# Performance work log

Measured on AMD Instinct MI355X. Metric: run time of the kernel, lower is better.

Reference implementation:

```python
import jax, jax.numpy as jnp
import numpy as np

B, S, D, NH, NKV, HD, FF = 2, 2048, 2048, 16, 8, 128, 8192
EPS = 1e-6
ROPE_THETA = 10000.0


def rmsnorm(x, w):
    return x * jax.lax.rsqrt(jnp.mean(x * x, axis=-1, keepdims=True) + EPS) * w


def rotate_half(x):
    h = x.shape[-1] // 2
    return jnp.concatenate([-x[..., h:], x[..., :h]], axis=-1)


def setup_inputs() -> dict:
    key = jax.random.key(0)
    ks = jax.random.split(key, 32)
    sc = 0.02
    inp = {}
    inp['x'] = jax.random.normal(ks[0], (B, S, D), dtype=jnp.float32)
    pos = jnp.arange(S, dtype=jnp.float32)
    inv = 1.0 / (ROPE_THETA ** (jnp.arange(0, HD, 2, dtype=jnp.float32) / HD))
    fr = jnp.outer(pos, inv)
    emb = jnp.concatenate([fr, fr], axis=-1)  # [S, HD]
    inp['cos'] = jnp.broadcast_to(jnp.cos(emb)[None], (B, S, HD)).astype(jnp.float32)
    inp['sin'] = jnp.broadcast_to(jnp.sin(emb)[None], (B, S, HD)).astype(jnp.float32)
    inp['vision_token_mask'] = jax.random.randint(ks[1], (B, S), 0, 2) > 0
    inp['attn_norm_w'] = jnp.ones((D,), jnp.float32)
    inp['ffn_norm_w'] = jnp.ones((D,), jnp.float32)
    shapes = {
        'wq': (D, NH * HD), 'wk': (D, NKV * HD), 'wv': (D, NKV * HD), 'wo': (NH * HD, D),
        'mm_wq': (D, NH * HD), 'mm_wk': (D, NKV * HD), 'mm_wv': (D, NKV * HD), 'mm_wo': (NH * HD, D),
        'gate_w': (D, FF), 'up_w': (D, FF), 'down_w': (FF, D),
        'mm_gate_w': (D, FF), 'mm_up_w': (D, FF), 'mm_down_w': (FF, D),
    }
    for i, (name, shp) in enumerate(shapes.items()):
        inp[name] = jax.random.normal(ks[2 + i], shp, dtype=jnp.float32) * sc
    for name in ['q_norm_w', 'k_norm_w', 'mm_q_norm_w', 'mm_k_norm_w']:
        inp[name] = jnp.ones((HD,), jnp.float32)
    return inp


def gpt_block(x, cos, sin, mask, attn_norm_w, ffn_norm_w,
              wq, wk, wv, wo, mm_wq, mm_wk, mm_wv, mm_wo,
              q_norm_w, k_norm_w, mm_q_norm_w, mm_k_norm_w,
              gate_w, up_w, down_w, mm_gate_w, mm_up_w, mm_down_w):
    m2 = mask[..., None]            # [B,S,1]
    m4 = mask[:, :, None, None]     # [B,S,1,1]
    h = rmsnorm(x, attn_norm_w)
    # dual-path QKV: text tokens use plain weights, vision tokens use mm_* weights
    q_t = rmsnorm((h @ wq).reshape(B, S, NH, HD), q_norm_w)
    q_v = rmsnorm((h @ mm_wq).reshape(B, S, NH, HD), mm_q_norm_w)
    q = jnp.where(m4, q_v, q_t)
    k_t = rmsnorm((h @ wk).reshape(B, S, NKV, HD), k_norm_w)
    k_v = rmsnorm((h @ mm_wk).reshape(B, S, NKV, HD), mm_k_norm_w)
    k = jnp.where(m4, k_v, k_t)
    v = jnp.where(m2, h @ mm_wv, h @ wv).reshape(B, S, NKV, HD)
    # RoPE (unsqueeze over head dim)
    cu = cos[:, :, None, :]
    su = sin[:, :, None, :]
    q = q * cu + rotate_half(q) * su
    k = k * cu + rotate_half(k) * su
    # GQA repeat + causal attention
    rep = NH // NKV
    k_r = jnp.repeat(k, rep, axis=2)
    v_r = jnp.repeat(v, rep, axis=2)
    scale = 1.0 / jnp.sqrt(jnp.float32(HD))
    scores = jnp.einsum('bqhd,bkhd->bhqk', q, k_r) * scale
    causal = jnp.tril(jnp.ones((S, S), bool))
    scores = jnp.where(causal, scores, jnp.float32(-1e30))
    p = jax.nn.softmax(scores, axis=-1)
    attn = jnp.einsum('bhqk,bkhd->bqhd', p, v_r).reshape(B, S, NH * HD)
    attn_out = jnp.where(m2, attn @ mm_wo, attn @ wo)
    h2 = x + attn_out
    # dual-path SwiGLU FFN
    g = rmsnorm(h2, ffn_norm_w)
    ff_t = (jax.nn.silu(g @ gate_w) * (g @ up_w)) @ down_w
    ff_v = (jax.nn.silu(g @ mm_gate_w) * (g @ mm_up_w)) @ mm_down_w
    return h2 + jnp.where(m2, ff_v, ff_t)


def reference(x, cos, sin, vision_token_mask, attn_norm_w, ffn_norm_w,
              wq, wk, wv, wo, mm_wq, mm_wk, mm_wv, mm_wo,
              q_norm_w, k_norm_w, mm_q_norm_w, mm_k_norm_w,
              gate_w, up_w, down_w, mm_gate_w, mm_up_w, mm_down_w):
    return gpt_block(x, cos, sin, vision_token_mask, attn_norm_w, ffn_norm_w,
                     wq, wk, wv, wo, mm_wq, mm_wk, mm_wv, mm_wo,
                     q_norm_w, k_norm_w, mm_q_norm_w, mm_k_norm_w,
                     gate_w, up_w, down_w, mm_gate_w, mm_up_w, mm_down_w)
```

## Files before the change

### kernel.cpp

```cpp
#include <hip/hip_runtime.h>

typedef unsigned short u16;
typedef __bf16 bf16x8 __attribute__((ext_vector_type(8)));
typedef float f32x4 __attribute__((ext_vector_type(4)));

__device__ __forceinline__ u16 f2bf(float f) {
    unsigned u = __builtin_bit_cast(unsigned, f);
    u += 0x7fffu + ((u >> 16) & 1u);
    return (u16)(u >> 16);
}
__device__ __forceinline__ float bf2f(u16 v) {
    unsigned u = ((unsigned)v) << 16;
    return __builtin_bit_cast(float, u);
}
__device__ __forceinline__ void glds16(const void* g, void* l) {
    __builtin_amdgcn_global_load_lds(
        (const __attribute__((address_space(1))) unsigned*)g,
        (__attribute__((address_space(3))) unsigned*)l, 16, 0, 0);
}

__device__ __forceinline__ void xcd_map(int bid, int nloc, int TM, int& tm, int& tn)
{
    const int xcd = bid & 7;
    int l = bid >> 3;
    const int per = nloc << 3;
    const int fullC = TM >> 3;
    const int lFull = fullC * per;
    int c, tn_l, tmIn;
    if (l < lFull) { c = l / per; int r = l - c * per; tn_l = r >> 3; tmIn = r & 7; }
    else { int r = l - lFull; int sc = TM - (fullC << 3); c = fullC; tn_l = r / sc; tmIn = r % sc; }
    tm = (c << 3) + tmIn;
    tn = xcd * nloc + tn_l;
}

__global__ __launch_bounds__(1024) void build_perm(
    const int* __restrict__ mask, int* __restrict__ perm, int* __restrict__ counts)
{
    __shared__ int sc[1024];
    int t = threadIdx.x;
    int m[4], cnt = 0;
#pragma unroll
    for (int j = 0; j < 4; j++) {
        m[j] = mask[t * 4 + j] != 0;
        cnt += (m[j] == 0);
    }
    sc[t] = cnt;
    __syncthreads();
    for (int off = 1; off < 1024; off <<= 1) {
        int v = (t >= off) ? sc[t - off] : 0;
        __syncthreads();
        sc[t] += v;
        __syncthreads();
    }
    int totT = sc[1023];
    int exT = sc[t] - cnt;
    int exV = t * 4 - exT;
    int pT = exT, pV = totT + exV;
#pragma unroll
    for (int j = 0; j < 4; j++) {
        if (m[j] == 0) perm[pT++] = t * 4 + j;
        else           perm[pV++] = t * 4 + j;
    }
    if (t == 0) { counts[0] = totT; counts[1] = 4096 - totT; }
}

__global__ __launch_bounds__(256) void transpose_bf16(
    const float* __restrict__ W, u16* __restrict__ Wt, int Kd, int Nd)
{
    __shared__ float tile[32][33];
    int k0 = blockIdx.x * 32, n0 = blockIdx.y * 32;
    int tx = threadIdx.x, ty = threadIdx.y;
#pragma unroll
    for (int i = 0; i < 32; i += 8)
        tile[ty + i][tx] = W[(long)(k0 + ty + i) * Nd + n0 + tx];
    __syncthreads();
#pragma unroll
    for (int i = 0; i < 32; i += 8)
        Wt[(long)(n0 + ty + i) * Kd + k0 + tx] = f2bf(tile[tx][ty + i]);
}

__global__ __launch_bounds__(256) void rms_x(
    const float* __restrict__ x, const float* __restrict__ w, u16* __restrict__ out)
{
    long row = blockIdx.x;
    int t = threadIdx.x, wave = t >> 6, lane = t & 63;
    const float4* x4 = (const float4*)(x + row * 2048);
    float4 a = x4[2 * t], b = x4[2 * t + 1];
    float ss = a.x*a.x + a.y*a.y + a.z*a.z + a.w*a.w
             + b.x*b.x + b.y*b.y + b.z*b.z + b.w*b.w;
#pragma unroll
    for (int m = 1; m < 64; m <<= 1) ss += __shfl_xor(ss, m);
    __shared__ float red[4];
    if (lane == 0) red[wave] = ss;
    __syncthreads();
    float tot = red[0] + red[1] + red[2] + red[3];
    float inv = rsqrtf(tot * (1.0f / 2048.0f) + 1e-6f);
    const float4* w4 = (const float4*)w;
    float4 wa = w4[2 * t], wb = w4[2 * t + 1];
    u16* op = out + row * 2048 + t * 8;
    op[0] = f2bf(a.x * inv * wa.x); op[1] = f2bf(a.y * inv * wa.y);
    op[2] = f2bf(a.z * inv * wa.z); op[3] = f2bf(a.w * inv * wa.w);
    op[4] = f2bf(b.x * inv * wb.x); op[5] = f2bf(b.y * inv * wb.y);
    op[6] = f2bf(b.z * inv * wb.z); op[7] = f2bf(b.w * inv * wb.w);
}

template <int EPI, bool PG, bool PC>
__global__ __launch_bounds__(512, 4) void gemm32(
    const u16* __restrict__ A, const u16* __restrict__ Bt0, const u16* __restrict__ Bt1,
    void* __restrict__ Cv,
    const int* __restrict__ perm, const int* __restrict__ counts, int N, int K)
{
    extern __shared__ u16 lds[];
    int tm, tn;
    xcd_map(blockIdx.x, N >> 11, 33, tm, tn);
    const int nT = counts[0];
    const int tT = (nT + 127) >> 7, tV = (4096 - nT + 127) >> 7;
    if (tm >= tT + tV) return;
    const bool vis = tm >= tT;
    const u16* Bt = vis ? Bt1 : Bt0;
    const int rowbase = vis ? nT + (tm - tT) * 128 : tm * 128;
    const int rowlim = vis ? 4096 : nT;
    const int tid = threadIdx.x;
    const int wave = tid >> 6, lane = tid & 63;
    const int wrbase = (wave >> 2) * 64, wcbase = (wave & 3) * 64;
    const int lr = lane & 15, lg = lane >> 4;
    const int n0 = tn * 256;
    const int t4 = tid >> 2, sp = tid & 3;
    const char* aSrc;
    const char* bSrc[2];
    {
        int r = t4;
        int gr = rowbase + r; gr = gr < 4095 ? gr : 4095;
        long ar = PG ? perm[gr] : gr;
        aSrc = (const char*)A + ar * (long)K * 2 + ((sp ^ (r & 3)) << 4);
    }
#pragma unroll
    for (int c = 0; c < 2; c++) {
        int r = c * 128 + t4;
        bSrc[c] = (const char*)Bt + (long)(n0 + r) * K * 2 + ((sp ^ (r & 3)) << 4);
    }
    auto stage = [&](int kt, int bu) {
        char* ab = (char*)lds + bu * 24576;
        long ko = (long)kt * 64;
        glds16(aSrc + ko, ab + tid * 16);
#pragma unroll
        for (int c = 0; c < 2; c++)
            glds16(bSrc[c] + ko, ab + 8192 + c * 8192 + tid * 16);
    };
    auto ldA = [&](int bu, int mi) -> bf16x8 {
        const char* ab = (const char*)lds + bu * 24576;
        int row = wrbase + mi * 16 + lr;
        return *(const bf16x8*)(ab + row * 64 + ((lg ^ (row & 3)) << 4));
    };
    auto ldB = [&](int bu, int ni) -> bf16x8 {
        const char* bb = (const char*)lds + bu * 24576 + 8192;
        int row = wcbase + ni * 16 + lr;
        return *(const bf16x8*)(bb + row * 64 + ((lg ^ (row & 3)) << 4));
    };

    f32x4 acc[4][4] = {};
    const int nkt = K >> 5;
    stage(0, 0);
    stage(1, 1);
    for (int kt = 0; kt < nkt; ++kt) {
        const int bu = kt % 3;
        if (kt == nkt - 1) asm volatile("s_waitcnt vmcnt(0)" ::: "memory");
        else               asm volatile("s_waitcnt vmcnt(3)" ::: "memory");
        __builtin_amdgcn_s_barrier();
        if (kt + 2 < nkt) stage(kt + 2, (kt + 2) % 3);
        bf16x8 af[4], bq[4];
#pragma unroll
        for (int i = 0; i < 4; i++) af[i] = ldA(bu, i);
#pragma unroll
        for (int j = 0; j < 4; j++) bq[j] = ldB(bu, j);
        __builtin_amdgcn_s_setprio(1);
#pragma unroll
        for (int i = 0; i < 4; i++)
#pragma unroll
            for (int j = 0; j < 4; j++)
                acc[i][j] = __builtin_amdgcn_mfma_f32_16x16x32_bf16(
                    af[i], bq[j], acc[i][j], 0, 0, 0);
        __builtin_amdgcn_s_setprio(0);
    }
#pragma unroll
    for (int mi = 0; mi < 4; mi++)
#pragma unroll
        for (int r = 0; r < 4; r++) {
            int gr = rowbase + wrbase + mi * 16 + lg * 4 + r;
            if (gr >= rowlim) continue;
            long crow = PC ? (long)perm[gr] : (long)gr;
#pragma unroll
            for (int ni = 0; ni < 4; ni++) {
                long col = n0 + wcbase + ni * 16 + lr;
                ((u16*)Cv)[crow * (long)N + col] = f2bf(acc[mi][ni][r]);
            }
        }
}

__global__ __launch_bounds__(512, 4) void gemm_gu(
    const u16* __restrict__ A,
    const u16* __restrict__ Bg0, const u16* __restrict__ Bg1,
    const u16* __restrict__ Bu0, const u16* __restrict__ Bu1,
    u16* __restrict__ C,
    const int* __restrict__ perm, const int* __restrict__ counts, int N, int K)
{
    extern __shared__ u16 lds[];
    int tm, tn;
    xcd_map(blockIdx.x, N >> 10, 33, tm, tn);
    const int nT = counts[0];
    const int tT = (nT + 127) >> 7, tV = (4096 - nT + 127) >> 7;
    if (tm >= tT + tV) return;
    const bool vis = tm >= tT;
    const u16* Bg = vis ? Bg1 : Bg0;
    const u16* Bu = vis ? Bu1 : Bu0;
    const int rowbase = vis ? nT + (tm - tT) * 128 : tm * 128;
    const int rowlim = vis ? 4096 : nT;
    const int tid = threadIdx.x;
    const int wave = tid >> 6, lane = tid & 63;
    const int wrbase = (wave >> 2) * 64, wcbase = (wave & 3) * 32;
    const int lr = lane & 15, lg = lane >> 4;
    const int n0 = tn * 128;
    const int t4 = tid >> 2, sp = tid & 3;
    const char *aSrc, *gSrc, *uSrc;
    {
        int r = t4;
        int gr = rowbase + r; gr = gr < 4095 ? gr : 4095;
        long ar = (long)perm[gr];
        aSrc = (const char*)A + ar * (long)K * 2 + ((sp ^ (r & 3)) << 4);
        gSrc = (const char*)Bg + (long)(n0 + r) * K * 2 + ((sp ^ (r & 3)) << 4);
        uSrc = (const char*)Bu + (long)(n0 + r) * K * 2 + ((sp ^ (r & 3)) << 4);
    }
    auto stage = [&](int kt, int bu) {
        char* ab = (char*)lds + bu * 24576;
        long ko = (long)kt * 64;
        glds16(aSrc + ko, ab + tid * 16);
        glds16(gSrc + ko, ab + 8192 + tid * 16);
        glds16(uSrc + ko, ab + 16384 + tid * 16);
    };
    auto ldA = [&](int bu, int mi) -> bf16x8 {
        const char* ab = (const char*)lds + bu * 24576;
        int row = wrbase + mi * 16 + lr;
        return *(const bf16x8*)(ab + row * 64 + ((lg ^ (row & 3)) << 4));
    };
    auto ldGU = [&](int bu, int sub, int ni) -> bf16x8 {
        const char* p = (const char*)lds + bu * 24576 + 8192 + sub * 8192;
        int row = wcbase + ni * 16 + lr;
        return *(const bf16x8*)(p + row * 64 + ((lg ^ (row & 3)) << 4));
    };

    f32x4 accg[4][2] = {}, accu[4][2] = {};
    const int nkt = K >> 5;
    stage(0, 0);
    stage(1, 1);
    for (int kt = 0; kt < nkt; ++kt) {
        const int bu = kt % 3;
        if (kt == nkt - 1) asm volatile("s_waitcnt vmcnt(0)" ::: "memory");
        else               asm volatile("s_waitcnt vmcnt(3)" ::: "memory");
        __builtin_amdgcn_s_barrier();
        if (kt + 2 < nkt) stage(kt + 2, (kt + 2) % 3);
        bf16x8 af[4], bg[2], bv[2];
#pragma unroll
        for (int i = 0; i < 4; i++) af[i] = ldA(bu, i);
#pragma unroll
        for (int j = 0; j < 2; j++) {
            bg[j] = ldGU(bu, 0, j);
            bv[j] = ldGU(bu, 1, j);
        }
        __builtin_amdgcn_s_setprio(1);
#pragma unroll
        for (int i = 0; i < 4; i++)
#pragma unroll
            for (int j = 0; j < 2; j++) {
                accg[i][j] = __builtin_amdgcn_mfma_f32_16x16x32_bf16(
                    af[i], bg[j], accg[i][j], 0, 0, 0);
                accu[i][j] = __builtin_amdgcn_mfma_f32_16x16x32_bf16(
                    af[i], bv[j], accu[i][j], 0, 0, 0);
            }
        __builtin_amdgcn_s_setprio(0);
    }
#pragma unroll
    for (int mi = 0; mi < 4; mi++)
#pragma unroll
        for (int r = 0; r < 4; r++) {
            int gr = rowbase + wrbase + mi * 16 + lg * 4 + r;
            if (gr >= rowlim) continue;
#pragma unroll
            for (int ni = 0; ni < 2; ni++) {
                long col = n0 + wcbase + ni * 16 + lr;
                float g = accg[mi][ni][r], u = accu[mi][ni][r];
                C[(long)gr * N + col] = f2bf(g / (1.0f + __expf(-g)) * u);
            }
        }
}

template <int EPI, bool PG, bool PC>
__global__ __launch_bounds__(512, 2) void gemmk(
    const u16* __restrict__ A, const u16* __restrict__ Bt0, const u16* __restrict__ Bt1,
    void* __restrict__ Cv, const float* __restrict__ resid,
    const int* __restrict__ perm, const int* __restrict__ counts, int N, int K)
{
    extern __shared__ u16 lds[];
    int tm, tn;
    xcd_map(blockIdx.x, N >> 11, 33, tm, tn);
    const int nT = counts[0];
    const int tT = (nT + 127) >> 7, tV = (4096 - nT + 127) >> 7;
    if (tm >= tT + tV) return;
    const bool vis = tm >= tT;
    const u16* Bt = vis ? Bt1 : Bt0;
    const int rowbase = vis ? nT + (tm - tT) * 128 : tm * 128;
    const int rowlim = vis ? 4096 : nT;
    const int tid = threadIdx.x;
    const int wave = tid >> 6, lane = tid & 63;
    const int wrbase = (wave >> 2) * 64, wcbase = (wave & 3) * 64;
    const int lr = lane & 15, lg = lane >> 4;
    const int n0 = tn * 256;
    const int t8 = tid >> 3, sp = tid & 7;
    const char* aSrc[2];
    const char* bSrc[4];
#pragma unroll
    for (int c = 0; c < 2; c++) {
        int r = c * 64 + t8;
        int gr = rowbase + r; gr = gr < 4095 ? gr : 4095;
        long ar = PG ? perm[gr] : gr;
        aSrc[c] = (const char*)A + ar * (long)K * 2 + ((sp ^ (r & 7)) << 4);
    }
#pragma unroll
    for (int c = 0; c < 4; c++) {
        int r = c * 64 + t8;
        bSrc[c] = (const char*)Bt + (long)(n0 + r) * K * 2 + ((sp ^ (r & 7)) << 4);
    }
    auto stage = [&](int kt, int bu) {
        char* ab = (char*)lds + bu * 49152;
        char* bb = ab + 16384;
        long ko = (long)kt * 128;
#pragma unroll
        for (int c = 0; c < 2; c++)
            glds16(aSrc[c] + ko, ab + c * 8192 + tid * 16);
#pragma unroll
        for (int c = 0; c < 4; c++)
            glds16(bSrc[c] + ko, bb + c * 8192 + tid * 16);
    };
    auto ldA = [&](int bu, int mi, int kk) -> bf16x8 {
        const char* ab = (const char*)lds + bu * 49152;
        int row = wrbase + mi * 16 + lr;
        int sl = kk * 4 + lg;
        return *(const bf16x8*)(ab + row * 128 + ((sl ^ (row & 7)) << 4));
    };
    auto ldB = [&](int bu, int ni, int kk) -> bf16x8 {
        const char* bb = (const char*)lds + bu * 49152 + 16384;
        int row = wcbase + ni * 16 + lr;
        int sl = kk * 4 + lg;
        return *(const bf16x8*)(bb + row * 128 + ((sl ^ (row & 7)) << 4));
    };

    f32x4 acc[4][4] = {};
    const int nkt = K >> 6;
    stage(0, 0);
    stage(1, 1);
    for (int kt = 0; kt < nkt; ++kt) {
        const int bu = kt % 3;
        if (kt == nkt - 1) asm volatile("s_waitcnt vmcnt(0)" ::: "memory");
        else               asm volatile("s_waitcnt vmcnt(6)" ::: "memory");
        __builtin_amdgcn_s_barrier();
        if (kt + 2 < nkt) stage(kt + 2, (kt + 2) % 3);
#pragma unroll
        for (int kk = 0; kk < 2; kk++) {
            bf16x8 af[4], bq[4];
#pragma unroll
            for (int i = 0; i < 4; i++) af[i] = ldA(bu, i, kk);
#pragma unroll
            for (int j = 0; j < 4; j++) bq[j] = ldB(bu, j, kk);
            __builtin_amdgcn_s_setprio(1);
#pragma unroll
            for (int i = 0; i < 4; i++)
#pragma unroll
                for (int j = 0; j < 4; j++)
                    acc[i][j] = __builtin_amdgcn_mfma_f32_16x16x32_bf16(
                        af[i], bq[j], acc[i][j], 0, 0, 0);
            __builtin_amdgcn_s_setprio(0);
        }
    }
#pragma unroll
    for (int mi = 0; mi < 4; mi++)
#pragma unroll
        for (int r = 0; r < 4; r++) {
            int gr = rowbase + wrbase + mi * 16 + lg * 4 + r;
            if (gr >= rowlim) continue;
            long crow = PC ? (long)perm[gr] : (long)gr;
#pragma unroll
            for (int ni = 0; ni < 4; ni++) {
                long col = n0 + wcbase + ni * 16 + lr;
                long idx = crow * (long)N + col;
                float v = acc[mi][ni][r];
                if (EPI == 1)      ((u16*)Cv)[idx] = f2bf(v);
                else if (EPI == 2) ((float*)Cv)[idx] = resid[idx] + v;
            }
        }
}

__global__ __launch_bounds__(256) void qk_fuse(
    const u16* __restrict__ p, const int* __restrict__ mask,
    const float* __restrict__ cs, const float* __restrict__ sn,
    const float* __restrict__ nwt, const float* __restrict__ nwv,
    u16* __restrict__ out, int H, int stride)
{
    int wave = threadIdx.x >> 6, lane = threadIdx.x & 63;
    int gw = blockIdx.x * 4 + wave;
    int tok = gw / H, h = gw % H;
    int b = tok >> 11, s = tok & 2047;
    const u16* src = p + (long)tok * stride + h * 128;
    const float* w = mask[tok] ? nwv : nwt;
    int d = lane * 2;
    float yx = bf2f(src[d]), yy = bf2f(src[d + 1]);
    float ss = yx * yx + yy * yy;
#pragma unroll
    for (int m = 1; m < 64; m <<= 1) ss += __shfl_xor(ss, m);
    float inv = rsqrtf(ss * (1.0f / 128.0f) + 1e-6f);
    float y0 = yx * inv * w[d], y1 = yy * inv * w[d + 1];
    float o0 = __shfl_xor(y0, 32), o1 = __shfl_xor(y1, 32);
    float sgn = (lane < 32) ? -1.0f : 1.0f;
    const float* cp = cs + (long)tok * 128 + d;
    const float* sp = sn + (long)tok * 128 + d;
    float r0 = y0 * cp[0] + sgn * o0 * sp[0];
    float r1 = y1 * cp[1] + sgn * o1 * sp[1];
    u16* op = out + (((long)b * H + h) * 2048 + s) * 128 + d;
    op[0] = f2bf(r0); op[1] = f2bf(r1);
}

__global__ __launch_bounds__(256) void v_fuse(
    const u16* __restrict__ vsrc, u16* __restrict__ outv, int stride)
{
    __shared__ u16 tile[32][33];
    int s0 = blockIdx.x * 32, d0 = blockIdx.y * 32;
    int bkv = blockIdx.z, b = bkv >> 3, kv = bkv & 7;
    int tx = threadIdx.x, ty = threadIdx.y;
#pragma unroll
    for (int i = 0; i < 32; i += 8) {
        long tok = (long)b * 2048 + s0 + ty + i;
        tile[ty + i][tx] = vsrc[tok * stride + kv * 128 + d0 + tx];
    }
    __syncthreads();
#pragma unroll
    for (int i = 0; i < 32; i += 8)
        outv[(((long)b * 8 + kv) * 128 + d0 + ty + i) * 2048 + s0 + tx] =
            tile[tx][ty + i];
}

__global__ __launch_bounds__(256) void attn_fwd(
    const u16* __restrict__ q, const u16* __restrict__ k,
    const u16* __restrict__ v, u16* __restrict__ out)
{
    __shared__ u16 Ks[32 * 128];
    __shared__ u16 Vs[128 * 32];
    __shared__ u16 Ps[4][16][40];
    const int tid = threadIdx.x, wave = tid >> 6, lane = tid & 63;
    const int lr = lane & 15, lg = lane >> 4;
    const int b = blockIdx.z, h = blockIdx.y, q0 = blockIdx.x * 64;
    const int kvh = h >> 1;
    const u16* qp = q + (((long)b * 16 + h) * 2048 + q0 + wave * 16) * 128;
    bf16x8 qf[4];
#pragma unroll
    for (int f = 0; f < 4; f++)
        qf[f] = *(const bf16x8*)(qp + (long)lr * 128 + f * 32 + lg * 8);
    const char* kbase = (const char*)(k + ((long)b * 8 + kvh) * 2048 * 128);
    const char* vbase = (const char*)(v + ((long)b * 8 + kvh) * 128 * 2048);
    f32x4 o[8] = {};
    float lsum[4] = {};
    const float sc2 = 0.08838834764831845f * 1.44269504088896f;
    const float MB = 16.5f;
    const int ntiles = (q0 + 64) >> 5;
    for (int t = 0; t < ntiles; ++t) {
        int kv0 = t * 32;
        __syncthreads();
#pragma unroll
        for (int j = 0; j < 2; j++) {
            int L = (j * 4 + wave) * 1024 + lane * 16;
            {
                int row = L >> 8, cb = L & 255;
                glds16(kbase + (long)(kv0 + row) * 256 + (cb ^ ((row & 7) << 4)),
                       (char*)Ks + (j * 4 + wave) * 1024);
            }
            {
                int row = L >> 6, cb = L & 63;
                glds16(vbase + (long)row * 4096 + kv0 * 2 + (cb ^ ((row & 3) << 4)),
                       (char*)Vs + (j * 4 + wave) * 1024);
            }
        }
        __syncthreads();
        f32x4 s[2] = {};
#pragma unroll
        for (int sub = 0; sub < 2; ++sub)
#pragma unroll
            for (int f = 0; f < 4; ++f) {
                int row = sub * 16 + lr;
                int cb = (f * 64 + lg * 16) ^ ((row & 7) << 4);
                bf16x8 kf = *(const bf16x8*)((const char*)Ks + row * 256 + cb);
                s[sub] = __builtin_amdgcn_mfma_f32_16x16x32_bf16(qf[f], kf, s[sub], 0, 0, 0);
            }
#pragma unroll
        for (int r = 0; r < 4; r++) {
            int rowg = q0 + wave * 16 + lg * 4 + r;
            float s0 = s[0][r] * sc2 - MB; if (kv0 + lr > rowg)      s0 = -1e30f;
            float s1 = s[1][r] * sc2 - MB; if (kv0 + 16 + lr > rowg) s1 = -1e30f;
            float p0 = exp2f(s0), p1 = exp2f(s1);
            lsum[r] += p0 + p1;
            int prow = lg * 4 + r;
            Ps[wave][prow][lr] = f2bf(p0);
            Ps[wave][prow][16 + lr] = f2bf(p1);
        }
        bf16x8 pf = *(const bf16x8*)&Ps[wave][lr][lg * 8];
#pragma unroll
        for (int ni = 0; ni < 8; ni++) {
            int row = ni * 16 + lr;
            int cb = (lg * 16) ^ ((row & 3) << 4);
            bf16x8 vf = *(const bf16x8*)((const char*)Vs + row * 64 + cb);
            o[ni] = __builtin_amdgcn_mfma_f32_16x16x32_bf16(pf, vf, o[ni], 0, 0, 0);
        }
    }
#pragma unroll
    for (int r = 0; r < 4; r++)
#pragma unroll
        for (int mm = 1; mm < 16; mm <<= 1) lsum[r] += __shfl_xor(lsum[r], mm);
#pragma unroll
    for (int ni = 0; ni < 8; ni++)
#pragma unroll
        for (int r = 0; r < 4; r++) {
            long row = (long)b * 2048 + q0 + wave * 16 + lg * 4 + r;
            out[row * 2048 + h * 128 + ni * 16 + lr] = f2bf(o[ni][r] / lsum[r]);
        }
}

extern "C" void kernel_launch(void* const* d_in, const int* in_sizes, int n_in,
                              void* d_out, int out_size, void* d_ws, size_t ws_size,
                              hipStream_t stream)
{
    const float* x    = (const float*)d_in[0];
    const float* cosp = (const float*)d_in[1];
    const float* sinp = (const float*)d_in[2];
    const int*   mask = (const int*)d_in[3];
    const float* anw  = (const float*)d_in[4];
    const float* fnw  = (const float*)d_in[5];
    const float* wq   = (const float*)d_in[6];
    const float* wk   = (const float*)d_in[7];
    const float* wv   = (const float*)d_in[8];
    const float* wo   = (const float*)d_in[9];
    const float* mwq  = (const float*)d_in[10];
    const float* mwk  = (const float*)d_in[11];
    const float* mwv  = (const float*)d_in[12];
    const float* mwo  = (const float*)d_in[13];
    const float* gw   = (const float*)d_in[14];
    const float* uw   = (const float*)d_in[15];
    const float* dw   = (const float*)d_in[16];
    const float* mgw  = (const float*)d_in[17];
    const float* muw  = (const float*)d_in[18];
    const float* mdw  = (const float*)d_in[19];
    const float* qnw  = (const float*)d_in[20];
    const float* knw  = (const float*)d_in[21];
    const float* mqnw = (const float*)d_in[22];
    const float* mknw = (const float*)d_in[23];

    char* base = (char*)d_ws;
    u16* wA0   = (u16*)(base);
    u16* wA1   = (u16*)(base + (32u << 20));
    u16* wB0   = (u16*)(base + (64u << 20));
    u16* wB1   = (u16*)(base + (96u << 20));
    u16* hbf   = (u16*)(base + (64u << 20));
    u16* qkv   = (u16*)(base + (80u << 20));
    u16* qb    = (u16*)(base + (112u << 20));
    u16* kb    = (u16*)(base + (128u << 20));
    u16* vb    = (u16*)(base + (136u << 20));
    u16* attnb = (u16*)(base + (144u << 20));
    u16* e1    = (u16*)(base + (128u << 20));
    float* h2  = (float*)(base + (192u << 20));
    u16* gbf   = (u16*)(base + (224u << 20));
    int* perm  = (int*)(base + (240u << 20));
    int* cnts  = perm + 4096;

    hipFuncSetAttribute((const void*)&gemm32<1, true, true>,
                        hipFuncAttributeMaxDynamicSharedMemorySize, 73728);
    hipFuncSetAttribute((const void*)&gemm_gu,
                        hipFuncAttributeMaxDynamicSharedMemorySize, 73728);
    hipFuncSetAttribute((const void*)&gemmk<2, true, true>,
                        hipFuncAttributeMaxDynamicSharedMemorySize, 147456);
    hipFuncSetAttribute((const void*)&gemmk<2, false, true>,
                        hipFuncAttributeMaxDynamicSharedMemorySize, 147456);

    dim3 tb(32, 8);
    auto TR = [&](const float* w, u16* dst, int K, int N) {
        transpose_bf16<<<dim3(K / 32, N / 32), tb, 0, stream>>>(w, dst, K, N);
    };

    build_perm<<<1, 1024, 0, stream>>>(mask, perm, cnts);
    rms_x<<<4096, 256, 0, stream>>>(x, anw, hbf);

    TR(wq, wA0, 2048, 2048);
    TR(wk, wA0 + (long)2048 * 2048, 2048, 1024);
    TR(wv, wA0 + (long)3072 * 2048, 2048, 1024);
    TR(mwq, wA1, 2048, 2048);
    TR(mwk, wA1 + (long)2048 * 2048, 2048, 1024);
    TR(mwv, wA1 + (long)3072 * 2048, 2048, 1024);
    gemm32<1, true, true><<<528, 512, 73728, stream>>>(
        hbf, wA0, wA1, (void*)qkv, perm, cnts, 4096, 2048);

    qk_fuse<<<16384, 256, 0, stream>>>(qkv, mask, cosp, sinp, qnw, mqnw, qb, 16, 4096);
    qk_fuse<<<8192, 256, 0, stream>>>(qkv + 2048, mask, cosp, sinp, knw, mknw, kb, 8, 4096);
    v_fuse<<<dim3(64, 4, 16), tb, 0, stream>>>(qkv + 3072, vb, 4096);

    attn_fwd<<<dim3(32, 16, 2), 256, 0, stream>>>(qb, kb, vb, attnb);

    TR(wo, wA0, 2048, 2048); TR(mwo, wA1, 2048, 2048);
    gemmk<2, true, true><<<264, 512, 147456, stream>>>(
        attnb, wA0, wA1, (void*)h2, x, perm, cnts, 2048, 2048);

    rms_x<<<4096, 256, 0, stream>>>(h2, fnw, gbf);

    TR(gw, wA0, 2048, 8192); TR(mgw, wA1, 2048, 8192);
    TR(uw, wB0, 2048, 8192); TR(muw, wB1, 2048, 8192);
    gemm_gu<<<2112, 512, 73728, stream>>>(
        gbf, wA0, wA1, wB0, wB1, e1, perm, cnts, 8192, 2048);
    TR(dw, wA0, 8192, 2048); TR(mdw, wA1, 8192, 2048);
    gemmk<2, false, true><<<264, 512, 147456, stream>>>(
        e1, wA0, wA1, (void*)d_out, h2, perm, cnts, 2048, 8192);
}
```

Measured before the change: 1.118 ms.

## Vectorize weight transpose and use smaller-tile GEMM for down projection

The fp32-to-bf16 weight transpose now works on 64x64 tiles, loading float4 and storing 8 packed bf16 values per thread, to cut memory transactions. The down-projection GEMM moves from the large-tile gemmk kernel to a new gemmsq kernel. gemmsq uses 128x128 tiles, double-buffered 32 KB of LDS, a K-step of 32 and an occupancy hint of 4 blocks, and is launched with twice as many blocks. This is meant to fill the GPU better for N=2048. The trade-off is less data reuse per tile and more global traffic for the K=8192 reduction.

```diff
diff --git a/kernel.cpp b/kernel.cpp
--- a/kernel.cpp
+++ b/kernel.cpp
@@ -67,16 +67,28 @@
 __global__ __launch_bounds__(256) void transpose_bf16(
     const float* __restrict__ W, u16* __restrict__ Wt, int Kd, int Nd)
 {
-    __shared__ float tile[32][33];
-    int k0 = blockIdx.x * 32, n0 = blockIdx.y * 32;
-    int tx = threadIdx.x, ty = threadIdx.y;
-#pragma unroll
-    for (int i = 0; i < 32; i += 8)
-        tile[ty + i][tx] = W[(long)(k0 + ty + i) * Nd + n0 + tx];
+    __shared__ float tile[64][65];
+    int k0 = blockIdx.x * 64, n0 = blockIdx.y * 64;
+    int t = threadIdx.x;
+    int rr = t >> 4, cc = (t & 15) * 4;
+#pragma unroll
+    for (int i = 0; i < 4; i++) {
+        float4 v = *(const float4*)&W[(long)(k0 + i * 16 + rr) * Nd + n0 + cc];
+        tile[i * 16 + rr][cc]     = v.x;
+        tile[i * 16 + rr][cc + 1] = v.y;
+        tile[i * 16 + rr][cc + 2] = v.z;
+        tile[i * 16 + rr][cc + 3] = v.w;
+    }
     __syncthreads();
-#pragma unroll
-    for (int i = 0; i < 32; i += 8)
-        Wt[(long)(n0 + ty + i) * Kd + k0 + tx] = f2bf(tile[tx][ty + i]);
+    int nn = t >> 3, k8 = (t & 7) * 8;
+#pragma unroll
+    for (int i = 0; i < 2; i++) {
+        int n = i * 32 + nn;
+        u16 pk[8];
+#pragma unroll
+        for (int j = 0; j < 8; j++) pk[j] = f2bf(tile[k8 + j][n]);
+        *(uint4*)&Wt[(long)(n0 + n) * Kd + k0 + k8] = *(const uint4*)pk;
+    }
 }
 
 __global__ __launch_bounds__(256) void rms_x(
@@ -294,6 +306,90 @@
 }
 
 template <int EPI, bool PG, bool PC>
+__global__ __launch_bounds__(512, 4) void gemmsq(
+    const u16* __restrict__ A, const u16* __restrict__ Bt0, const u16* __restrict__ Bt1,
+    void* __restrict__ Cv, const float* __restrict__ resid,
+    const int* __restrict__ perm, const int* __restrict__ counts, int N, int K)
+{
+    extern __shared__ u16 lds[];
+    int tm, tn;
+    xcd_map(blockIdx.x, N >> 10, 33, tm, tn);
+    const int nT = counts[0];
+    const int tT = (nT + 127) >> 7, tV = (4096 - nT + 127) >> 7;
+    if (tm >= tT + tV) return;
+    const bool vis = tm >= tT;
+    const u16* Bt = vis ? Bt1 : Bt0;
+    const int rowbase = vis ? nT + (tm - tT) * 128 : tm * 128;
+    const int rowlim = vis ? 4096 : nT;
+    const int tid = threadIdx.x;
+    const int wave = tid >> 6, lane = tid & 63;
+    const int wrbase = (wave >> 2) * 64, wcbase = (wave & 3) * 32;
+    const int lr = lane & 15, lg = lane >> 4;
+    const int n0 = tn * 128;
+    const int t4 = tid >> 2, sp = tid & 3;
+    const char *aSrc, *bSrc;
+    {
+        int r = t4;
+        int gr = rowbase + r; gr = gr < 4095 ? gr : 4095;
+        long ar = PG ? (long)perm[gr] : (long)gr;
+        aSrc = (const char*)A + ar * (long)K * 2 + ((sp ^ (r & 3)) << 4);
+        bSrc = (const char*)Bt + (long)(n0 + r) * K * 2 + ((sp ^ (r & 3)) << 4);
+    }
+    auto stage = [&](int kt, int bu) {
+        char* ab = (char*)lds + bu * 16384;
+        long ko = (long)kt * 64;
+        glds16(aSrc + ko, ab + tid * 16);
+        glds16(bSrc + ko, ab + 8192 + tid * 16);
+    };
+    auto ldA = [&](int bu, int mi) -> bf16x8 {
+        const char* ab = (const char*)lds + bu * 16384;
+        int row = wrbase + mi * 16 + lr;
+        return *(const bf16x8*)(ab + row * 64 + ((lg ^ (row & 3)) << 4));
+    };
+    auto ldB = [&](int bu, int ni) -> bf16x8 {
+        const char* bb = (const char*)lds + bu * 16384 + 8192;
+        int row = wcbase + ni * 16 + lr;
+        return *(const bf16x8*)(bb + row * 64 + ((lg ^ (row & 3)) << 4));
+    };
+
+    f32x4 acc[4][2] = {};
+    const int nkt = K >> 5;
+    stage(0, 0);
+    for (int kt = 0; kt < nkt; ++kt) {
+        const int bu = kt & 1;
+        __syncthreads();
+        if (kt + 1 < nkt) stage(kt + 1, bu ^ 1);
+        bf16x8 af[4], bq[2];
+#pragma unroll
+        for (int i = 0; i < 4; i++) af[i] = ldA(bu, i);
+#pragma unroll
+        for (int j = 0; j < 2; j++) bq[j] = ldB(bu, j);
+        __builtin_amdgcn_s_setprio(1);
+#pragma unroll
+        for (int i = 0; i < 4; i++)
+#pragma unroll
+            for (int j = 0; j < 2; j++)
+                acc[i][j] = __builtin_amdgcn_mfma_f32_16x16x32_bf16(
+                    af[i], bq[j], acc[i][j], 0, 0, 0);
+        __builtin_amdgcn_s_setprio(0);
+    }
+#pragma unroll
+    for (int mi = 0; mi < 4; mi++)
+#pragma unroll
+        for (int r = 0; r < 4; r++) {
+            int gr = rowbase + wrbase + mi * 16 + lg * 4 + r;
+            if (gr >= rowlim) continue;
+            long crow = PC ? (long)perm[gr] : (long)gr;
+#pragma unroll
+            for (int ni = 0; ni < 2; ni++) {
+                long col = n0 + wcbase + ni * 16 + lr;
+                long idx = crow * (long)N + col;
+                ((float*)Cv)[idx] = resid[idx] + acc[mi][ni][r];
+            }
+        }
+}
+
+template <int EPI, bool PG, bool PC>
 __global__ __launch_bounds__(512, 2) void gemmk(
     const u16* __restrict__ A, const u16* __restrict__ Bt0, const u16* __restrict__ Bt1,
     void* __restrict__ Cv, const float* __restrict__ resid,
@@ -420,9 +516,9 @@
     float o0 = __shfl_xor(y0, 32), o1 = __shfl_xor(y1, 32);
     float sgn = (lane < 32) ? -1.0f : 1.0f;
     const float* cp = cs + (long)tok * 128 + d;
-    const float* sp = sn + (long)tok * 128 + d;
-    float r0 = y0 * cp[0] + sgn * o0 * sp[0];
-    float r1 = y1 * cp[1] + sgn * o1 * sp[1];
+    const float* spn = sn + (long)tok * 128 + d;
+    float r0 = y0 * cp[0] + sgn * o0 * spn[0];
+    float r1 = y1 * cp[1] + sgn * o1 * spn[1];
     u16* op = out + (((long)b * H + h) * 2048 + s) * 128 + d;
     op[0] = f2bf(r0); op[1] = f2bf(r1);
 }
@@ -582,12 +678,9 @@
                         hipFuncAttributeMaxDynamicSharedMemorySize, 73728);
     hipFuncSetAttribute((const void*)&gemmk<2, true, true>,
                         hipFuncAttributeMaxDynamicSharedMemorySize, 147456);
-    hipFuncSetAttribute((const void*)&gemmk<2, false, true>,
-                        hipFuncAttributeMaxDynamicSharedMemorySize, 147456);
-
-    dim3 tb(32, 8);
+
     auto TR = [&](const float* w, u16* dst, int K, int N) {
-        transpose_bf16<<<dim3(K / 32, N / 32), tb, 0, stream>>>(w, dst, K, N);
+        transpose_bf16<<<dim3(K / 64, N / 64), 256, 0, stream>>>(w, dst, K, N);
     };
 
     build_perm<<<1, 1024, 0, stream>>>(mask, perm, cnts);
@@ -604,7 +697,7 @@
 
     qk_fuse<<<16384, 256, 0, stream>>>(qkv, mask, cosp, sinp, qnw, mqnw, qb, 16, 4096);
     qk_fuse<<<8192, 256, 0, stream>>>(qkv + 2048, mask, cosp, sinp, knw, mknw, kb, 8, 4096);
-    v_fuse<<<dim3(64, 4, 16), tb, 0, stream>>>(qkv + 3072, vb, 4096);
+    v_fuse<<<dim3(64, 4, 16), dim3(32, 8), 0, stream>>>(qkv + 3072, vb, 4096);
 
     attn_fwd<<<dim3(32, 16, 2), 256, 0, stream>>>(qb, kb, vb, attnb);
 
@@ -619,6 +712,6 @@
     gemm_gu<<<2112, 512, 73728, stream>>>(
         gbf, wA0, wA1, wB0, wB1, e1, perm, cnts, 8192, 2048);
     TR(dw, wA0, 8192, 2048); TR(mdw, wA1, 8192, 2048);
-    gemmk<2, false, true><<<264, 512, 147456, stream>>>(
+    gemmsq<2, false, true><<<528, 512, 32768, stream>>>(
         e1, wA0, wA1, (void*)d_out, h2, perm, cnts, 2048, 8192);
 }
```

Result: faster. 1.033 ms (-7.6%).
